# Kernel tuning notes

Hardware: AMD Instinct MI355X
Metric: run time of the kernel (lower is better)

The kernel has to match this reference:

```python
import jax, jax.numpy as jnp
import numpy as np

SEQ, BATCH, IN_DIM, HID, OUT = 512, 256, 300, 256, 2


def setup_inputs() -> dict:
    key = jax.random.key(0)
    ks = jax.random.split(key, 7)
    s_ih = 1.0 / np.sqrt(HID)
    return {
        "x": jax.random.normal(ks[0], (SEQ, BATCH, IN_DIM), jnp.float32),
        "W_ih": jax.random.uniform(ks[1], (HID, IN_DIM), jnp.float32, -s_ih, s_ih),
        "W_hh": jax.random.uniform(ks[2], (HID, HID), jnp.float32, -s_ih, s_ih),
        "b_ih": jax.random.uniform(ks[3], (HID,), jnp.float32, -s_ih, s_ih),
        "b_hh": jax.random.uniform(ks[4], (HID,), jnp.float32, -s_ih, s_ih),
        "W_fc": jax.random.uniform(ks[5], (OUT, HID), jnp.float32, -s_ih, s_ih),
        "b_fc": jax.random.uniform(ks[6], (OUT,), jnp.float32, -s_ih, s_ih),
    }


def reference(x, W_ih, W_hh, b_ih, b_hh, W_fc, b_fc):
    # Precompute input projection for all timesteps at once: [T, B, H]
    xp = jnp.einsum('tbi,hi->tbh', x, W_ih) + b_ih + b_hh

    def step(h, xt):
        h_new = jnp.tanh(xt + h @ W_hh.T)
        return h_new, None

    h0 = jnp.zeros((x.shape[1], W_hh.shape[0]), x.dtype)
    hT, _ = jax.lax.scan(step, h0, xp)  # hT: [B, H]
    # Dropout(0.3) is identity in eval mode.
    logits = hT @ W_fc.T + b_fc  # [B, 2]
    return jax.nn.log_softmax(logits, axis=-1)
```

## Files before the change

### kernel.cpp

```cpp
#include <hip/hip_runtime.h>
#include <hip/hip_bf16.h>
#include <cstdint>
#include <cstddef>

#define SEQ 512
#define BATCH 256
#define IN_DIM 300
#define HID 256

typedef __attribute__((ext_vector_type(8))) short bf16x8;
typedef __attribute__((ext_vector_type(4))) float f32x4;

__device__ __forceinline__ unsigned short f2bf(float f) {
  union { float f; unsigned int u; } v; v.f = f;
  unsigned int u = v.u;
  return (unsigned short)((u + 0x7fffu + ((u >> 16) & 1u)) >> 16);
}
__device__ __forceinline__ unsigned short f2bf_fast(float f) {
  union { float f; unsigned int u; } v; v.f = f;
  return (unsigned short)((v.u + 0x8000u) >> 16);
}
__device__ __forceinline__ float bitsf(unsigned int u) {
  union { unsigned int u; float f; } v; v.u = u; return v.f;
}
__device__ __forceinline__ bf16x8 cvt8(float a0,float a1,float a2,float a3,
                                       float a4,float a5,float a6,float a7) {
  union { __hip_bfloat162 h2[4]; bf16x8 v; } c;
  c.h2[0] = __float22bfloat162_rn(make_float2(a0, a1));
  c.h2[1] = __float22bfloat162_rn(make_float2(a2, a3));
  c.h2[2] = __float22bfloat162_rn(make_float2(a4, a5));
  c.h2[3] = __float22bfloat162_rn(make_float2(a6, a7));
  return c.v;
}

__global__ __launch_bounds__(256) void conv_wih(const float* __restrict__ w,
                                                unsigned short* __restrict__ w_bf) {
  int idx = blockIdx.x * 256 + threadIdx.x;
  int n = idx / 320, k = idx - n * 320;
  float v = (k < IN_DIM) ? w[n * IN_DIM + k] : 0.f;
  w_bf[idx] = f2bf(v);
}

__global__ __launch_bounds__(256) void gemm_xp(const float* __restrict__ x,
    const unsigned short* __restrict__ w_bf, const float* __restrict__ b_ih,
    const float* __restrict__ b_hh, unsigned int* __restrict__ xp2)
{
  __shared__ unsigned short a_lds[64][40];
  __shared__ unsigned short w_lds[256][40];
  const int tid  = threadIdx.x;
  const int wave = tid >> 6;
  const int lane = tid & 63;
  const int l15  = lane & 15;
  const int quad = lane >> 4;
  const long m0 = (long)blockIdx.x * 64;

  f32x4 acc[4][4];
  #pragma unroll
  for (int mt = 0; mt < 4; ++mt)
    #pragma unroll
    for (int nt = 0; nt < 4; ++nt) acc[mt][nt] = (f32x4){0.f, 0.f, 0.f, 0.f};

  const int ar = tid >> 2;
  const int ac = (tid & 3) * 8;

  float av[8];
  uint2 wv[8];
  {
    const float* src = x + (size_t)(m0 + ar) * IN_DIM + ac;
    float2 p0 = *(const float2*)(src + 0);
    float2 p1 = *(const float2*)(src + 2);
    float2 p2 = *(const float2*)(src + 4);
    float2 p3 = *(const float2*)(src + 6);
    av[0]=p0.x; av[1]=p0.y; av[2]=p1.x; av[3]=p1.y;
    av[4]=p2.x; av[5]=p2.y; av[6]=p3.x; av[7]=p3.y;
    #pragma unroll
    for (int i = 0; i < 8; ++i) {
      int e = tid + i * 256;
      wv[i] = *(const uint2*)(w_bf + (e >> 3) * 320 + (e & 7) * 4);
    }
  }

  for (int kc = 0; kc < 10; ++kc) {
    *(bf16x8*)&a_lds[ar][ac] = cvt8(av[0],av[1],av[2],av[3],av[4],av[5],av[6],av[7]);
    #pragma unroll
    for (int i = 0; i < 8; ++i) {
      int e = tid + i * 256;
      *(uint2*)&w_lds[e >> 3][(e & 7) * 4] = wv[i];
    }
    __syncthreads();
    if (kc < 9) {
      const int k0 = (kc + 1) * 32;
      const float* src = x + (size_t)(m0 + ar) * IN_DIM + (k0 + ac);
      if (k0 + ac + 8 <= IN_DIM) {
        float2 p0 = *(const float2*)(src + 0);
        float2 p1 = *(const float2*)(src + 2);
        float2 p2 = *(const float2*)(src + 4);
        float2 p3 = *(const float2*)(src + 6);
        av[0]=p0.x; av[1]=p0.y; av[2]=p1.x; av[3]=p1.y;
        av[4]=p2.x; av[5]=p2.y; av[6]=p3.x; av[7]=p3.y;
      } else {
        #pragma unroll
        for (int j = 0; j < 8; ++j) av[j] = (k0 + ac + j < IN_DIM) ? src[j] : 0.f;
      }
      #pragma unroll
      for (int i = 0; i < 8; ++i) {
        int e = tid + i * 256;
        wv[i] = *(const uint2*)(w_bf + (e >> 3) * 320 + k0 + (e & 7) * 4);
      }
    }
    bf16x8 afr[4], bfr[4];
    #pragma unroll
    for (int mt = 0; mt < 4; ++mt)
      afr[mt] = *(const bf16x8*)&a_lds[mt*16 + l15][quad*8];
    #pragma unroll
    for (int nt = 0; nt < 4; ++nt)
      bfr[nt] = *(const bf16x8*)&w_lds[wave*64 + nt*16 + l15][quad*8];
    #pragma unroll
    for (int mt = 0; mt < 4; ++mt)
      #pragma unroll
      for (int nt = 0; nt < 4; ++nt)
        acc[mt][nt] = __builtin_amdgcn_mfma_f32_16x16x32_bf16(afr[mt], bfr[nt], acc[mt][nt], 0, 0, 0);
    __syncthreads();
  }
  const int t = (int)(blockIdx.x >> 2);
  #pragma unroll
  for (int nt = 0; nt < 4; ++nt) {
    const int n = wave*64 + nt*16 + l15;
    const float kb = 2.0f * (b_ih[n] + b_hh[n]);
    const int tid_lo = (wave*2 + (nt>>1))*64 + (nt&1)*16 + l15;
    #pragma unroll
    for (int mt = 0; mt < 4; ++mt) {
      const int g = ((int)(blockIdx.x & 3))*16 + mt*4 + quad;
      const size_t base = ((size_t)t*64 + g)*512;
      float y0 = fmaf(2.0f, acc[mt][nt][0], kb);
      float y1 = fmaf(2.0f, acc[mt][nt][1], kb);
      float y2 = fmaf(2.0f, acc[mt][nt][2], kb);
      float y3 = fmaf(2.0f, acc[mt][nt][3], kb);
      union { __hip_bfloat162 h2; unsigned int u; } p01, p23;
      p01.h2 = __float22bfloat162_rn(make_float2(y0, y1));
      p23.h2 = __float22bfloat162_rn(make_float2(y2, y3));
      xp2[base + tid_lo]      = p01.u;
      xp2[base + tid_lo + 32] = p23.u;
    }
  }
}

__global__ __launch_bounds__(512) void rnn_scan(const float* __restrict__ W_hh,
    const unsigned int* __restrict__ xp2, float* __restrict__ hT)
{
  __shared__ alignas(16) unsigned short hbuf[2][4 * 272];
  const int tid  = threadIdx.x;
  const int wave = tid >> 6;
  const int lane = tid & 63;
  const int l15  = lane & 15;
  const int quad = lane >> 4;
  const int g = blockIdx.x;
  const int c0 = wave * 32;

  bf16x8 wf[2][8];
  #pragma unroll
  for (int nt = 0; nt < 2; ++nt) {
    const int n = c0 + nt*16 + l15;
    #pragma unroll
    for (int kc = 0; kc < 8; ++kc) {
      const float* src = W_hh + n*HID + kc*32 + quad*8;
      float4 p0 = *(const float4*)src;
      float4 p1 = *(const float4*)(src + 4);
      wf[nt][kc] = cvt8(p0.x,p0.y,p0.z,p0.w,p1.x,p1.y,p1.z,p1.w);
    }
  }

  const int rb    = (quad >> 1) * 2;
  const int col_e = c0 + (quad & 1) * 16 + l15;
  const int abase = (l15 & 3) * 272 + quad * 8;

  for (int i = tid; i < 4 * 272; i += 512) hbuf[0][i] = 0;

  const unsigned int* xbase = xp2 + (size_t)g * 512 + tid;

  __syncthreads();

  unsigned int xq[16];
  for (int tc = 0; tc < SEQ / 16; ++tc) {
    const unsigned int* pb = xbase + (size_t)tc * 16 * 32768;
    #pragma unroll
    for (int j = 0; j < 16; ++j)
      xq[j] = pb[(size_t)j * 32768];
    #pragma unroll
    for (int j = 0; j < 16; ++j) {
      const int cur = j & 1;
      bf16x8 afr[8];
      #pragma unroll
      for (int kc = 0; kc < 8; ++kc)
        afr[kc] = *(const bf16x8*)&hbuf[cur][abase + kc*32];
      f32x4 a0A = (f32x4){0.f,0.f,0.f,0.f}, a0B = a0A, a1A = a0A, a1B = a0A;
      #pragma unroll
      for (int kc = 0; kc < 8; kc += 2) {
        a0A = __builtin_amdgcn_mfma_f32_16x16x32_bf16(afr[kc],   wf[0][kc],   a0A, 0, 0, 0);
        a1A = __builtin_amdgcn_mfma_f32_16x16x32_bf16(afr[kc],   wf[1][kc],   a1A, 0, 0, 0);
        a0B = __builtin_amdgcn_mfma_f32_16x16x32_bf16(afr[kc+1], wf[0][kc+1], a0B, 0, 0, 0);
        a1B = __builtin_amdgcn_mfma_f32_16x16x32_bf16(afr[kc+1], wf[1][kc+1], a1B, 0, 0, 0);
      }
      f32x4 acc0 = a0A + a0B;
      f32x4 acc1 = a1A + a1B;
      f32x4 a = (quad & 1) ? acc1 : acc0;
      float s0 = (quad >> 1) ? a[2] : a[0];
      float s1 = (quad >> 1) ? a[3] : a[1];
      float xv0 = bitsf(xq[j] << 16);
      float xv1 = bitsf(xq[j] & 0xffff0000u);
      float y0 = fmaf(2.0f, s0, xv0);
      float y1 = fmaf(2.0f, s1, xv1);
      float h0 = fmaf(-2.0f, __builtin_amdgcn_rcpf(__expf(y0) + 1.0f), 1.0f);
      float h1 = fmaf(-2.0f, __builtin_amdgcn_rcpf(__expf(y1) + 1.0f), 1.0f);
      if (j < 15 || tc < SEQ/16 - 1) {
        hbuf[1 - cur][ rb      * 272 + col_e] = f2bf_fast(h0);
        hbuf[1 - cur][(rb + 1) * 272 + col_e] = f2bf_fast(h1);
      } else {
        hT[(size_t)(g*4 + rb    ) * HID + col_e] = h0;
        hT[(size_t)(g*4 + rb + 1) * HID + col_e] = h1;
      }
      __syncthreads();
    }
  }
}

__global__ __launch_bounds__(64) void fc_head(const float* __restrict__ hT,
    const float* __restrict__ W_fc, const float* __restrict__ b_fc,
    float* __restrict__ out)
{
  const int b = blockIdx.x;
  const int l = threadIdx.x;
  float s0 = 0.f, s1 = 0.f;
  #pragma unroll
  for (int j0 = 0; j0 < HID; j0 += 64) {
    float h = hT[(size_t)b * HID + j0 + l];
    s0 += h * W_fc[j0 + l];
    s1 += h * W_fc[HID + j0 + l];
  }
  #pragma unroll
  for (int off = 32; off > 0; off >>= 1) {
    s0 += __shfl_xor(s0, off, 64);
    s1 += __shfl_xor(s1, off, 64);
  }
  if (l == 0) {
    float l0 = s0 + b_fc[0], l1 = s1 + b_fc[1];
    float m = fmaxf(l0, l1);
    float lse = m + logf(expf(l0 - m) + expf(l1 - m));
    out[b*2 + 0] = l0 - lse;
    out[b*2 + 1] = l1 - lse;
  }
}

extern "C" void kernel_launch(void* const* d_in, const int* in_sizes, int n_in,
                              void* d_out, int out_size, void* d_ws, size_t ws_size,
                              hipStream_t stream) {
  const float* x    = (const float*)d_in[0];
  const float* W_ih = (const float*)d_in[1];
  const float* W_hh = (const float*)d_in[2];
  const float* b_ih = (const float*)d_in[3];
  const float* b_hh = (const float*)d_in[4];
  const float* W_fc = (const float*)d_in[5];
  const float* b_fc = (const float*)d_in[6];
  float* out = (float*)d_out;

  const size_t xp_bytes = (size_t)SEQ * BATCH * HID * 2;
  const size_t wb_bytes = (size_t)256 * 320 * 2;
  const size_t ht_bytes = (size_t)BATCH * HID * 4;
  if (ws_size < xp_bytes + wb_bytes + ht_bytes) return;

  char* ws = (char*)d_ws;
  unsigned int*   xp2  = (unsigned int*)ws;
  unsigned short* w_bf = (unsigned short*)(ws + xp_bytes);
  float*          hT   = (float*)(ws + xp_bytes + wb_bytes);

  hipLaunchKernelGGL(conv_wih, dim3(320),  dim3(256), 0, stream, W_ih, w_bf);
  hipLaunchKernelGGL(gemm_xp,  dim3(2048), dim3(256), 0, stream, x, w_bf, b_ih, b_hh, xp2);
  hipLaunchKernelGGL(rnn_scan, dim3(64),   dim3(512), 0, stream, W_hh, xp2, hT);
  hipLaunchKernelGGL(fc_head,  dim3(BATCH), dim3(64), 0, stream, hT, W_fc, b_fc, out);
}
```

Baseline: 501.6 us.

## Fuse W_ih conversion into GEMM, remap recurrent output layout, deepen xp prefetch

```diff
diff --git a/kernel.cpp b/kernel.cpp
--- a/kernel.cpp
+++ b/kernel.cpp
@@ -11,17 +11,13 @@
 typedef __attribute__((ext_vector_type(8))) short bf16x8;
 typedef __attribute__((ext_vector_type(4))) float f32x4;
 
-__device__ __forceinline__ unsigned short f2bf(float f) {
-  union { float f; unsigned int u; } v; v.f = f;
-  unsigned int u = v.u;
-  return (unsigned short)((u + 0x7fffu + ((u >> 16) & 1u)) >> 16);
-}
-__device__ __forceinline__ unsigned short f2bf_fast(float f) {
-  union { float f; unsigned int u; } v; v.f = f;
-  return (unsigned short)((v.u + 0x8000u) >> 16);
-}
 __device__ __forceinline__ float bitsf(unsigned int u) {
   union { unsigned int u; float f; } v; v.u = u; return v.f;
+}
+__device__ __forceinline__ unsigned int pk2(float a, float b) {
+  union { __hip_bfloat162 h2; unsigned int u; } p;
+  p.h2 = __float22bfloat162_rn(make_float2(a, b));
+  return p.u;
 }
 __device__ __forceinline__ bf16x8 cvt8(float a0,float a1,float a2,float a3,
                                        float a4,float a5,float a6,float a7) {
@@ -33,16 +29,8 @@
   return c.v;
 }
 
-__global__ __launch_bounds__(256) void conv_wih(const float* __restrict__ w,
-                                                unsigned short* __restrict__ w_bf) {
-  int idx = blockIdx.x * 256 + threadIdx.x;
-  int n = idx / 320, k = idx - n * 320;
-  float v = (k < IN_DIM) ? w[n * IN_DIM + k] : 0.f;
-  w_bf[idx] = f2bf(v);
-}
-
 __global__ __launch_bounds__(256) void gemm_xp(const float* __restrict__ x,
-    const unsigned short* __restrict__ w_bf, const float* __restrict__ b_ih,
+    const float* __restrict__ W_ih, const float* __restrict__ b_ih,
     const float* __restrict__ b_hh, unsigned int* __restrict__ xp2)
 {
   __shared__ unsigned short a_lds[64][40];
@@ -64,7 +52,7 @@
   const int ac = (tid & 3) * 8;
 
   float av[8];
-  uint2 wv[8];
+  float4 wv[8];
   {
     const float* src = x + (size_t)(m0 + ar) * IN_DIM + ac;
     float2 p0 = *(const float2*)(src + 0);
@@ -76,7 +64,7 @@
     #pragma unroll
     for (int i = 0; i < 8; ++i) {
       int e = tid + i * 256;
-      wv[i] = *(const uint2*)(w_bf + (e >> 3) * 320 + (e & 7) * 4);
+      wv[i] = *(const float4*)(W_ih + (e >> 3) * IN_DIM + (e & 7) * 4);
     }
   }
 
@@ -85,7 +73,10 @@
     #pragma unroll
     for (int i = 0; i < 8; ++i) {
       int e = tid + i * 256;
-      *(uint2*)&w_lds[e >> 3][(e & 7) * 4] = wv[i];
+      union { unsigned int u[2]; uint2 d; } pk;
+      pk.u[0] = pk2(wv[i].x, wv[i].y);
+      pk.u[1] = pk2(wv[i].z, wv[i].w);
+      *(uint2*)&w_lds[e >> 3][(e & 7) * 4] = pk.d;
     }
     __syncthreads();
     if (kc < 9) {
@@ -105,7 +96,10 @@
       #pragma unroll
       for (int i = 0; i < 8; ++i) {
         int e = tid + i * 256;
-        wv[i] = *(const uint2*)(w_bf + (e >> 3) * 320 + k0 + (e & 7) * 4);
+        int kk = k0 + (e & 7) * 4;
+        wv[i] = (kk + 4 <= IN_DIM)
+              ? *(const float4*)(W_ih + (e >> 3) * IN_DIM + kk)
+              : make_float4(0.f, 0.f, 0.f, 0.f);
       }
     }
     bf16x8 afr[4], bfr[4];
@@ -123,24 +117,20 @@
     __syncthreads();
   }
   const int t = (int)(blockIdx.x >> 2);
-  #pragma unroll
-  for (int nt = 0; nt < 4; ++nt) {
-    const int n = wave*64 + nt*16 + l15;
-    const float kb = 2.0f * (b_ih[n] + b_hh[n]);
-    const int tid_lo = (wave*2 + (nt>>1))*64 + (nt&1)*16 + l15;
-    #pragma unroll
-    for (int mt = 0; mt < 4; ++mt) {
-      const int g = ((int)(blockIdx.x & 3))*16 + mt*4 + quad;
-      const size_t base = ((size_t)t*64 + g)*512;
-      float y0 = fmaf(2.0f, acc[mt][nt][0], kb);
-      float y1 = fmaf(2.0f, acc[mt][nt][1], kb);
-      float y2 = fmaf(2.0f, acc[mt][nt][2], kb);
-      float y3 = fmaf(2.0f, acc[mt][nt][3], kb);
-      union { __hip_bfloat162 h2; unsigned int u; } p01, p23;
-      p01.h2 = __float22bfloat162_rn(make_float2(y0, y1));
-      p23.h2 = __float22bfloat162_rn(make_float2(y2, y3));
-      xp2[base + tid_lo]      = p01.u;
-      xp2[base + tid_lo + 32] = p23.u;
+  const float kb0 = 2.0f * (b_ih[wave*64 +  0 + l15] + b_hh[wave*64 +  0 + l15]);
+  const float kb1 = 2.0f * (b_ih[wave*64 + 16 + l15] + b_hh[wave*64 + 16 + l15]);
+  const float kb2 = 2.0f * (b_ih[wave*64 + 32 + l15] + b_hh[wave*64 + 32 + l15]);
+  const float kb3 = 2.0f * (b_ih[wave*64 + 48 + l15] + b_hh[wave*64 + 48 + l15]);
+  #pragma unroll
+  for (int mt = 0; mt < 4; ++mt) {
+    const int g = ((int)(blockIdx.x & 3))*16 + mt*4 + quad;
+    const size_t base = ((size_t)t*64 + g)*512;
+    #pragma unroll
+    for (int r = 0; r < 4; ++r) {
+      unsigned int d0 = pk2(fmaf(2.0f, acc[mt][0][r], kb0), fmaf(2.0f, acc[mt][1][r], kb1));
+      unsigned int d1 = pk2(fmaf(2.0f, acc[mt][2][r], kb2), fmaf(2.0f, acc[mt][3][r], kb3));
+      xp2[base + (wave*2    )*64 + r*16 + l15] = d0;
+      xp2[base + (wave*2 + 1)*64 + r*16 + l15] = d1;
     }
   }
 }
@@ -163,16 +153,15 @@
     const int n = c0 + nt*16 + l15;
     #pragma unroll
     for (int kc = 0; kc < 8; ++kc) {
-      const float* src = W_hh + n*HID + kc*32 + quad*8;
+      const float* src = W_hh + n*HID + kc*32 + quad*4;
       float4 p0 = *(const float4*)src;
-      float4 p1 = *(const float4*)(src + 4);
-      wf[nt][kc] = cvt8(p0.x,p0.y,p0.z,p0.w,p1.x,p1.y,p1.z,p1.w);
-    }
-  }
-
-  const int rb    = (quad >> 1) * 2;
-  const int col_e = c0 + (quad & 1) * 16 + l15;
+      float4 p1 = *(const float4*)(src + 16);
+      wf[nt][kc] = cvt8(p0.x,p1.x,p0.y,p1.y,p0.z,p1.z,p0.w,p1.w);
+    }
+  }
+
   const int abase = (l15 & 3) * 272 + quad * 8;
+  const int wofs  = quad * 272 + wave * 32 + l15 * 2;
 
   for (int i = tid; i < 4 * 272; i += 512) hbuf[0][i] = 0;
 
@@ -180,44 +169,43 @@
 
   __syncthreads();
 
-  unsigned int xq[16];
-  for (int tc = 0; tc < SEQ / 16; ++tc) {
-    const unsigned int* pb = xbase + (size_t)tc * 16 * 32768;
-    #pragma unroll
-    for (int j = 0; j < 16; ++j)
+  unsigned int xq[32];
+  for (int tc = 0; tc < SEQ / 32; ++tc) {
+    const unsigned int* pb = xbase + (size_t)tc * 32 * 32768;
+    #pragma unroll
+    for (int j = 0; j < 32; ++j)
       xq[j] = pb[(size_t)j * 32768];
     #pragma unroll
-    for (int j = 0; j < 16; ++j) {
+    for (int j = 0; j < 32; ++j) {
       const int cur = j & 1;
       bf16x8 afr[8];
       #pragma unroll
       for (int kc = 0; kc < 8; ++kc)
         afr[kc] = *(const bf16x8*)&hbuf[cur][abase + kc*32];
-      f32x4 a0A = (f32x4){0.f,0.f,0.f,0.f}, a0B = a0A, a1A = a0A, a1B = a0A;
+      f32x4 c00 = (f32x4){0.f,0.f,0.f,0.f}, c01 = c00, c10 = c00, c11 = c00;
       #pragma unroll
       for (int kc = 0; kc < 8; kc += 2) {
-        a0A = __builtin_amdgcn_mfma_f32_16x16x32_bf16(afr[kc],   wf[0][kc],   a0A, 0, 0, 0);
-        a1A = __builtin_amdgcn_mfma_f32_16x16x32_bf16(afr[kc],   wf[1][kc],   a1A, 0, 0, 0);
-        a0B = __builtin_amdgcn_mfma_f32_16x16x32_bf16(afr[kc+1], wf[0][kc+1], a0B, 0, 0, 0);
-        a1B = __builtin_amdgcn_mfma_f32_16x16x32_bf16(afr[kc+1], wf[1][kc+1], a1B, 0, 0, 0);
-      }
-      f32x4 acc0 = a0A + a0B;
-      f32x4 acc1 = a1A + a1B;
-      f32x4 a = (quad & 1) ? acc1 : acc0;
-      float s0 = (quad >> 1) ? a[2] : a[0];
-      float s1 = (quad >> 1) ? a[3] : a[1];
+        c00 = __builtin_amdgcn_mfma_f32_16x16x32_bf16(afr[kc],   wf[0][kc],   c00, 0, 0, 0);
+        c10 = __builtin_amdgcn_mfma_f32_16x16x32_bf16(afr[kc],   wf[1][kc],   c10, 0, 0, 0);
+        c01 = __builtin_amdgcn_mfma_f32_16x16x32_bf16(afr[kc+1], wf[0][kc+1], c01, 0, 0, 0);
+        c11 = __builtin_amdgcn_mfma_f32_16x16x32_bf16(afr[kc+1], wf[1][kc+1], c11, 0, 0, 0);
+      }
+      const bool qb0 = (quad & 1) != 0, qb1 = (quad & 2) != 0;
+      float a0 = qb1 ? (qb0 ? c00[3]+c01[3] : c00[2]+c01[2])
+                     : (qb0 ? c00[1]+c01[1] : c00[0]+c01[0]);
+      float a1 = qb1 ? (qb0 ? c10[3]+c11[3] : c10[2]+c11[2])
+                     : (qb0 ? c10[1]+c11[1] : c10[0]+c11[0]);
       float xv0 = bitsf(xq[j] << 16);
       float xv1 = bitsf(xq[j] & 0xffff0000u);
-      float y0 = fmaf(2.0f, s0, xv0);
-      float y1 = fmaf(2.0f, s1, xv1);
+      float y0 = fmaf(2.0f, a0, xv0);
+      float y1 = fmaf(2.0f, a1, xv1);
       float h0 = fmaf(-2.0f, __builtin_amdgcn_rcpf(__expf(y0) + 1.0f), 1.0f);
       float h1 = fmaf(-2.0f, __builtin_amdgcn_rcpf(__expf(y1) + 1.0f), 1.0f);
-      if (j < 15 || tc < SEQ/16 - 1) {
-        hbuf[1 - cur][ rb      * 272 + col_e] = f2bf_fast(h0);
-        hbuf[1 - cur][(rb + 1) * 272 + col_e] = f2bf_fast(h1);
+      if (j < 31 || tc < SEQ/32 - 1) {
+        *(unsigned int*)&hbuf[1 - cur][wofs] = pk2(h0, h1);
       } else {
-        hT[(size_t)(g*4 + rb    ) * HID + col_e] = h0;
-        hT[(size_t)(g*4 + rb + 1) * HID + col_e] = h1;
+        hT[(size_t)(g*4 + quad) * HID + c0 + l15]      = h0;
+        hT[(size_t)(g*4 + quad) * HID + c0 + 16 + l15] = h1;
       }
       __syncthreads();
     }
@@ -264,17 +252,14 @@
   float* out = (float*)d_out;
 
   const size_t xp_bytes = (size_t)SEQ * BATCH * HID * 2;
-  const size_t wb_bytes = (size_t)256 * 320 * 2;
   const size_t ht_bytes = (size_t)BATCH * HID * 4;
-  if (ws_size < xp_bytes + wb_bytes + ht_bytes) return;
+  if (ws_size < xp_bytes + ht_bytes) return;
 
   char* ws = (char*)d_ws;
-  unsigned int*   xp2  = (unsigned int*)ws;
-  unsigned short* w_bf = (unsigned short*)(ws + xp_bytes);
-  float*          hT   = (float*)(ws + xp_bytes + wb_bytes);
-
-  hipLaunchKernelGGL(conv_wih, dim3(320),  dim3(256), 0, stream, W_ih, w_bf);
-  hipLaunchKernelGGL(gemm_xp,  dim3(2048), dim3(256), 0, stream, x, w_bf, b_ih, b_hh, xp2);
+  unsigned int* xp2 = (unsigned int*)ws;
+  float*        hT  = (float*)(ws + xp_bytes);
+
+  hipLaunchKernelGGL(gemm_xp,  dim3(2048), dim3(256), 0, stream, x, W_ih, b_ih, b_hh, xp2);
   hipLaunchKernelGGL(rnn_scan, dim3(64),   dim3(512), 0, stream, W_hh, xp2, hT);
   hipLaunchKernelGGL(fc_head,  dim3(BATCH), dim3(64), 0, stream, hT, W_fc, b_fc, out);
 }
```

Result: no change. 509.4 us (+1.6%).
